# Performance work log

Hardware: AMD Instinct MI355X
Metric: run time of the kernel (lower is better)

## Reference

```python
import jax, jax.numpy as jnp
import numpy as np

B, S, D, H = 2, 2048, 1024, 16
DK = D // H


def setup_inputs() -> dict:
    key = jax.random.key(0)
    ks = jax.random.split(key, 8)
    q = jax.random.normal(ks[0], (B, S, D), dtype=jnp.float32)
    k = jax.random.normal(ks[1], (B, S, D), dtype=jnp.float32)
    v = jax.random.normal(ks[2], (B, S, D), dtype=jnp.float32)
    mask = jax.random.randint(ks[3], (B, 1, S, S), 0, 2, dtype=jnp.int32)
    sc = 1.0 / np.sqrt(D)
    Wq = jax.random.normal(ks[4], (D, D), dtype=jnp.float32) * sc
    Wk = jax.random.normal(ks[5], (D, D), dtype=jnp.float32) * sc
    Wv = jax.random.normal(ks[6], (D, D), dtype=jnp.float32) * sc
    Wo = jax.random.normal(ks[7], (D, D), dtype=jnp.float32) * sc
    return {"q": q, "k": k, "v": v, "mask": mask, "Wq": Wq, "Wk": Wk, "Wv": Wv, "Wo": Wo}


def reference(q, k, v, mask, Wq, Wk, Wv, Wo):
    # Linear projections (torch Linear: x @ W.T; bias=False). Weights here stored
    # as [D, D] applied as x @ W (equivalent parameterization).
    query = q @ Wq  # [B,S,D]
    key = k @ Wk
    value = v @ Wv
    # split heads -> [B,H,S,DK]
    query = query.reshape(B, S, H, DK).transpose(0, 2, 1, 3)
    key = key.reshape(B, S, H, DK).transpose(0, 2, 1, 3)
    value = value.reshape(B, S, H, DK).transpose(0, 2, 1, 3)
    scores = jnp.einsum('bhqd,bhkd->bhqk', query, key) / jnp.sqrt(jnp.float32(DK))
    scores = jnp.where(mask == 0, jnp.float32(-1e9), scores)
    probs = jax.nn.softmax(scores, axis=-1)  # dropout p=0.0 -> identity
    x = jnp.einsum('bhqk,bhkd->bhqd', probs, value)
    x = x.transpose(0, 2, 1, 3).reshape(B, S, D)
    return x @ Wo
```

## Files before the change

kernel.cpp:

```cpp
#include <hip/hip_runtime.h>
#include <hip/hip_bf16.h>
#include <math.h>

#define B_ 2
#define S_ 2048
#define D_ 1024
#define H_ 16
#define DK_ 64
#define SW_ (S_ / 64)

typedef unsigned short u16;
typedef unsigned int u32;
typedef unsigned long long u64;
typedef __attribute__((ext_vector_type(8))) short short8;
typedef __attribute__((ext_vector_type(4))) float float4_;
typedef __attribute__((ext_vector_type(4))) unsigned int uint4_;

static __device__ inline u16 f_to_bf16(float f) {
    union { float f; u32 i; } x; x.f = f;
    u32 r = x.i + 0x7fff + ((x.i >> 16) & 1);
    return (u16)(r >> 16);
}

static __device__ __forceinline__ u32 cvtpk(float a, float b) {
    u32 r;
    asm("v_cvt_pk_bf16_f32 %0, %1, %2" : "=v"(r) : "v"(a), "v"(b));
    return r;
}

static __device__ __forceinline__ float fast_exp2(float x) {
#if __has_builtin(__builtin_amdgcn_exp2f)
    return __builtin_amdgcn_exp2f(x);
#else
    return exp2f(x);
#endif
}

static __device__ inline void gl_lds16(const u16* g, u16* l) {
    __builtin_amdgcn_global_load_lds((const __attribute__((address_space(1))) void*)g,
                                     (__attribute__((address_space(3))) void*)l, 16, 0, 0);
}

__global__ __launch_bounds__(256) void prep(const float* __restrict__ q,
                                            const float* __restrict__ k,
                                            const float* __restrict__ v,
                                            const int* __restrict__ mask,
                                            const float* __restrict__ W0,
                                            const float* __restrict__ W1,
                                            const float* __restrict__ W2,
                                            const float* __restrict__ W3,
                                            u16* __restrict__ qb, u16* __restrict__ kb,
                                            u16* __restrict__ vb,
                                            u16* __restrict__ T0, u16* __restrict__ T1,
                                            u16* __restrict__ T2, u16* __restrict__ T3,
                                            u64* __restrict__ mpk) {
    __shared__ float tile[32][33];
    int gx = blockIdx.x, tid = threadIdx.x;
    if (gx < 6144) {
        int z = gx >> 11;
        int bx = gx & 2047;
        const float* s = (z == 0) ? q : ((z == 1) ? k : v);
        u16* d = (z == 0) ? qb : ((z == 1) ? kb : vb);
        int i = (bx * 256 + tid) * 8;
        #pragma unroll
        for (int j = 0; j < 8; ++j) d[i + j] = f_to_bf16(s[i + j]);
    } else if (gx < 10240) {
        int g2 = gx - 6144;
        int z = g2 >> 10;
        int rem = g2 & 1023;
        const float* W = (z == 0) ? W0 : ((z == 1) ? W1 : ((z == 2) ? W2 : W3));
        u16* Wt = (z == 0) ? T0 : ((z == 1) ? T1 : ((z == 2) ? T2 : T3));
        int k0 = (rem >> 5) * 32, n0 = (rem & 31) * 32;
        int tx = tid & 31, ty = tid >> 5;
        #pragma unroll
        for (int i2 = 0; i2 < 4; ++i2) {
            int row = ty + i2 * 8;
            tile[row][tx] = W[(size_t)(k0 + row) * D_ + n0 + tx];
        }
        __syncthreads();
        #pragma unroll
        for (int i2 = 0; i2 < 4; ++i2) {
            int row = ty + i2 * 8;
            Wt[(size_t)(n0 + row) * D_ + k0 + tx] = f_to_bf16(tile[tx][row]);
        }
    } else {
        int g3 = gx - 10240;
        int wv = (g3 * 256 + tid) >> 6;
        int lane = tid & 63;
        #pragma unroll
        for (int i2 = 0; i2 < 8; ++i2) {
            int wd = wv * 8 + i2;
            u64 bits = __ballot(mask[(size_t)wd * 64 + lane] != 0);
            if (lane == 0) mpk[wd] = bits;
        }
    }
}

static __device__ __forceinline__ void gemm128_body(u16* lds,
                                                    const u16* __restrict__ A,
                                                    const u16* __restrict__ Bt,
                                                    int K, float4_ (&acc)[4][4]) {
    u16* ldsA = lds;
    u16* ldsB = lds + 8192;
    int tm = blockIdx.x, tn = blockIdx.y;
    int t = threadIdx.x, l = t & 63;
    int w = t >> 6, wr = w >> 1, wc = w & 1;
    int colL = l & 15, grp = l >> 4;
    int sw4 = (grp ^ ((colL >> 1) & 3)) << 3;
    int f0 = t, f1 = t + 256;
    int row0 = f0 >> 2, kc0 = (((f0 & 3) ^ ((f0 >> 3) & 3)) << 3);
    int row1 = f1 >> 2, kc1 = (((f1 & 3) ^ ((f1 >> 3) & 3)) << 3);
    const u16* gA0 = A  + (size_t)(tm * 128 + row0) * K + kc0;
    const u16* gA1 = A  + (size_t)(tm * 128 + row1) * K + kc1;
    const u16* gB0 = Bt + (size_t)(tn * 128 + row0) * K + kc0;
    const u16* gB1 = Bt + (size_t)(tn * 128 + row1) * K + kc1;

    #pragma unroll
    for (int mi = 0; mi < 4; ++mi)
        #pragma unroll
        for (int ni = 0; ni < 4; ++ni)
            acc[mi][ni] = (float4_){0.f, 0.f, 0.f, 0.f};

    gl_lds16(gA0, ldsA + f0 * 8);
    gl_lds16(gA1, ldsA + f1 * 8);
    gl_lds16(gB0, ldsB + f0 * 8);
    gl_lds16(gB1, ldsB + f1 * 8);

    for (int k0 = 0; k0 < K; k0 += 32) {
        int cur = (k0 >> 5) & 1;
        if (k0 + 32 < K) {
            int nb = (cur ^ 1) * 4096;
            gl_lds16(gA0 + k0 + 32, ldsA + nb + f0 * 8);
            gl_lds16(gA1 + k0 + 32, ldsA + nb + f1 * 8);
            gl_lds16(gB0 + k0 + 32, ldsB + nb + f0 * 8);
            gl_lds16(gB1 + k0 + 32, ldsB + nb + f1 * 8);
            asm volatile("s_waitcnt vmcnt(4)" ::: "memory");
        } else {
            asm volatile("s_waitcnt vmcnt(0)" ::: "memory");
        }
        __builtin_amdgcn_s_barrier();
        const u16* cA = ldsA + cur * 4096;
        const u16* cB = ldsB + cur * 4096;
        short8 a[4], b[4];
        #pragma unroll
        for (int mi = 0; mi < 4; ++mi)
            a[mi] = *(const short8*)&cA[(wr * 64 + mi * 16 + colL) * 32 + sw4];
        #pragma unroll
        for (int ni = 0; ni < 4; ++ni)
            b[ni] = *(const short8*)&cB[(wc * 64 + ni * 16 + colL) * 32 + sw4];
        #pragma unroll
        for (int mi = 0; mi < 4; ++mi)
            #pragma unroll
            for (int ni = 0; ni < 4; ++ni)
                acc[mi][ni] = __builtin_amdgcn_mfma_f32_16x16x32_bf16(a[mi], b[ni], acc[mi][ni], 0, 0, 0);
        __builtin_amdgcn_s_barrier();
    }
}

__global__ __launch_bounds__(256, 3) void gemm_qkv(const u16* __restrict__ qb,
                                                   const u16* __restrict__ kb,
                                                   const u16* __restrict__ vb,
                                                   const u16* __restrict__ Wqt,
                                                   const u16* __restrict__ Wkt,
                                                   const u16* __restrict__ Wvt,
                                                   u16* __restrict__ Qp,
                                                   u16* __restrict__ Kp,
                                                   u16* __restrict__ Vt) {
    __shared__ u16 lds[16384];
    int z = blockIdx.z;
    const u16* A  = (z == 0) ? qb  : ((z == 1) ? kb  : vb);
    const u16* Bt = (z == 0) ? Wqt : ((z == 1) ? Wkt : Wvt);
    float4_ acc[4][4];
    gemm128_body(lds, A, Bt, D_, acc);

    int tm = blockIdx.x, tn = blockIdx.y;
    int t = threadIdx.x, l = t & 63;
    int w = t >> 6, wr = w >> 1, wc = w & 1;
    int colL = l & 15, grp = l >> 4;

    if (z < 2) {
        u16* Y = (z == 0) ? Qp : Kp;
        float sc = (z == 0) ? (0.125f * 1.44269504f) : 1.0f;
        #pragma unroll
        for (int mi = 0; mi < 4; ++mi)
            #pragma unroll
            for (int ni = 0; ni < 4; ++ni)
                #pragma unroll
                for (int r = 0; r < 4; ++r)
                    Y[(size_t)(tm * 128 + wr * 64 + mi * 16 + grp * 4 + r) * D_
                      + tn * 128 + wc * 64 + ni * 16 + colL] = f_to_bf16(acc[mi][ni][r] * sc);
    } else {
        int tok_base = tm * 128 + wr * 64;
        int bb = tok_base >> 11;
        int s_hi = tok_base & (S_ - 1);
        #pragma unroll
        for (int mi = 0; mi < 4; ++mi)
            #pragma unroll
            for (int ni = 0; ni < 4; ++ni) {
                int n  = tn * 128 + wc * 64 + ni * 16 + colL;
                int hh = n >> 6, dk = n & 63;
                u16* vp = Vt + ((size_t)(bb * H_ + hh) * DK_ + dk) * S_ + s_hi;
                #pragma unroll
                for (int r = 0; r < 4; ++r) {
                    int m = mi * 16 + grp * 4 + r;
                    int mp_ = ((m >> 5) & 1) * 32 + ((m >> 2) & 3) * 8 + ((m >> 4) & 1) * 4 + (m & 3);
                    vp[mp_] = f_to_bf16(acc[mi][ni][r]);
                }
            }
    }
}

__global__ __launch_bounds__(256, 3) void gemm_out(const u16* __restrict__ Xa,
                                                   const u16* __restrict__ Wot,
                                                   float* __restrict__ out) {
    __shared__ u16 lds[16384];
    float4_ acc[4][4];
    gemm128_body(lds, Xa, Wot, D_, acc);

    int tm = blockIdx.x, tn = blockIdx.y;
    int t = threadIdx.x, l = t & 63;
    int w = t >> 6, wr = w >> 1, wc = w & 1;
    int colL = l & 15, grp = l >> 4;
    #pragma unroll
    for (int mi = 0; mi < 4; ++mi)
        #pragma unroll
        for (int ni = 0; ni < 4; ++ni)
            #pragma unroll
            for (int r = 0; r < 4; ++r)
                out[(size_t)(tm * 128 + wr * 64 + mi * 16 + grp * 4 + r) * D_
                    + tn * 128 + wc * 64 + ni * 16 + colL] = acc[mi][ni][r];
}

__global__ __launch_bounds__(256, 2) void attn128(const u16* __restrict__ Qp,
                                                  const u16* __restrict__ Kp,
                                                  const u16* __restrict__ Vt,
                                                  const u64* __restrict__ mp,
                                                  u16* __restrict__ Xa) {
    __shared__ u16 ldsK[2 * 128 * 64];
    __shared__ u16 ldsV[2 * 2 * 64 * 64];

    int bid0 = blockIdx.x;
    int bid = ((bid0 & 7) << 6) | (bid0 >> 3);
    int qt = bid & 15, h = (bid >> 4) & 15, b = bid >> 8;
    int t = threadIdx.x, l = t & 63, w = t >> 6;
    int colL = l & 15, grp = l >> 4;

    const u16* qbA = Qp + (size_t)(b * S_ + qt * 128 + w * 32 + colL) * D_ + h * DK_;
    const u16* qbB = qbA + (size_t)16 * D_;
    short8 qfA0 = *(const short8*)(qbA + grp * 8);
    short8 qfA1 = *(const short8*)(qbA + 32 + grp * 8);
    short8 qfB0 = *(const short8*)(qbB + grp * 8);
    short8 qfB1 = *(const short8*)(qbB + 32 + grp * 8);

    const u16* gK[4];
    const u16* gV[4];
    int fofs[4];
    #pragma unroll
    for (int i = 0; i < 4; ++i) {
        int f = t + 256 * i;
        fofs[i] = f * 8;
        int krow = f >> 3, kch = (((f & 7) ^ (krow & 7)) << 3);
        gK[i] = Kp + (size_t)(b * S_ + krow) * D_ + h * DK_ + kch;
        int hreg = f >> 9, fp = f & 511;
        int vrow = fp >> 3, vch = (((fp & 7) ^ (vrow & 7)) << 3);
        gV[i] = Vt + ((size_t)(b * H_ + h) * DK_ + vrow) * S_ + hreg * 64 + vch;
    }

    int sw8 = (grp ^ (colL & 7)) << 3;

    short8 onesb;
    #pragma unroll
    for (int j = 0; j < 8; ++j) onesb[j] = (short)0x3F80;

    float4_ laccA = (float4_){0.f, 0.f, 0.f, 0.f};
    float4_ laccB = (float4_){0.f, 0.f, 0.f, 0.f};
    float4_ oA[4], oB[4];
    #pragma unroll
    for (int nt = 0; nt < 4; ++nt) {
        oA[nt] = (float4_){0.f, 0.f, 0.f, 0.f};
        oB[nt] = (float4_){0.f, 0.f, 0.f, 0.f};
    }

    const u64* mrA = mp + (size_t)(b * S_ + qt * 128 + w * 32 + colL) * SW_;
    const u64* mrB = mrA + (size_t)16 * SW_;

    #pragma unroll
    for (int i = 0; i < 4; ++i) {
        gl_lds16(gK[i], ldsK + fofs[i]);
        gl_lds16(gV[i], ldsV + fofs[i]);
    }

    for (int kt = 0; kt < S_; kt += 128) {
        int cur = (kt >> 7) & 1;

        u64 mwA0 = mrA[(kt >> 6)];
        u64 mwA1 = mrA[(kt >> 6) + 1];
        u64 mwB0 = mrB[(kt >> 6)];
        u64 mwB1 = mrB[(kt >> 6) + 1];

        if (kt + 128 < S_) {
            int nb = (cur ^ 1) * 8192;
            #pragma unroll
            for (int i = 0; i < 4; ++i) {
                gl_lds16(gK[i] + (size_t)(kt + 128) * D_, ldsK + nb + fofs[i]);
                gl_lds16(gV[i] + (kt + 128),              ldsV + nb + fofs[i]);
            }
            asm volatile("s_waitcnt vmcnt(12)" ::: "memory");
        } else {
            asm volatile("s_waitcnt vmcnt(4)" ::: "memory");
        }
        __builtin_amdgcn_s_barrier();

        const u16* K_ = ldsK + cur * 8192;
        const u16* V_ = ldsV + cur * 8192;

        float4_ sA[8], sB[8];
        __builtin_amdgcn_s_setprio(1);
        #pragma unroll
        for (int nt = 0; nt < 8; ++nt) {
            int ro = (nt * 16 + colL) * 64;
            short8 kf0 = *(const short8*)&K_[ro + sw8];
            short8 kf1 = *(const short8*)&K_[ro + (sw8 ^ 32)];
            sA[nt] = (float4_){0.f, 0.f, 0.f, 0.f};
            sA[nt] = __builtin_amdgcn_mfma_f32_16x16x32_bf16(kf0, qfA0, sA[nt], 0, 0, 0);
            sA[nt] = __builtin_amdgcn_mfma_f32_16x16x32_bf16(kf1, qfA1, sA[nt], 0, 0, 0);
            sB[nt] = (float4_){0.f, 0.f, 0.f, 0.f};
            sB[nt] = __builtin_amdgcn_mfma_f32_16x16x32_bf16(kf0, qfB0, sB[nt], 0, 0, 0);
            sB[nt] = __builtin_amdgcn_mfma_f32_16x16x32_bf16(kf1, qfB1, sB[nt], 0, 0, 0);
        }
        __builtin_amdgcn_s_setprio(0);

        u64 mshA0 = mwA0 >> (grp * 4), mshA1 = mwA1 >> (grp * 4);
        u64 mshB0 = mwB0 >> (grp * 4), mshB1 = mwB1 >> (grp * 4);
        #pragma unroll
        for (int nt = 0; nt < 8; ++nt) {
            u32 bitsA = ((u32)((nt < 4 ? mshA0 : mshA1) >> ((nt & 3) * 16))) & 15u;
            u32 bitsB = ((u32)((nt < 4 ? mshB0 : mshB1) >> ((nt & 3) * 16))) & 15u;
            #pragma unroll
            for (int r = 0; r < 4; ++r) {
                float pA = fast_exp2(sA[nt][r]);
                float pB = fast_exp2(sB[nt][r]);
                u32 keepA = 0u - ((bitsA >> r) & 1u);
                u32 keepB = 0u - ((bitsB >> r) & 1u);
                union { float f; u32 i; } ua, ub;
                ua.f = pA; ua.i &= keepA; sA[nt][r] = ua.f;
                ub.f = pB; ub.i &= keepB; sB[nt][r] = ub.f;
            }
        }

        short8 pfA[4], pfB[4];
        #pragma unroll
        for (int j = 0; j < 4; ++j) {
            uint4_ Ax = { cvtpk(sA[2 * j][0], sA[2 * j][1]), cvtpk(sA[2 * j][2], sA[2 * j][3]),
                          cvtpk(sA[2 * j + 1][0], sA[2 * j + 1][1]), cvtpk(sA[2 * j + 1][2], sA[2 * j + 1][3]) };
            pfA[j] = __builtin_bit_cast(short8, Ax);
            uint4_ Bx = { cvtpk(sB[2 * j][0], sB[2 * j][1]), cvtpk(sB[2 * j][2], sB[2 * j][3]),
                          cvtpk(sB[2 * j + 1][0], sB[2 * j + 1][1]), cvtpk(sB[2 * j + 1][2], sB[2 * j + 1][3]) };
            pfB[j] = __builtin_bit_cast(short8, Bx);
        }

        __builtin_amdgcn_s_setprio(1);
        #pragma unroll
        for (int nt = 0; nt < 4; ++nt) {
            int ro = (nt * 16 + colL) * 64;
            short8 vf0 = *(const short8*)&V_[ro + sw8];
            short8 vf1 = *(const short8*)&V_[ro + (sw8 ^ 32)];
            short8 vf2 = *(const short8*)&V_[4096 + ro + sw8];
            short8 vf3 = *(const short8*)&V_[4096 + ro + (sw8 ^ 32)];
            oA[nt] = __builtin_amdgcn_mfma_f32_16x16x32_bf16(pfA[0], vf0, oA[nt], 0, 0, 0);
            oA[nt] = __builtin_amdgcn_mfma_f32_16x16x32_bf16(pfA[1], vf1, oA[nt], 0, 0, 0);
            oA[nt] = __builtin_amdgcn_mfma_f32_16x16x32_bf16(pfA[2], vf2, oA[nt], 0, 0, 0);
            oA[nt] = __builtin_amdgcn_mfma_f32_16x16x32_bf16(pfA[3], vf3, oA[nt], 0, 0, 0);
            oB[nt] = __builtin_amdgcn_mfma_f32_16x16x32_bf16(pfB[0], vf0, oB[nt], 0, 0, 0);
            oB[nt] = __builtin_amdgcn_mfma_f32_16x16x32_bf16(pfB[1], vf1, oB[nt], 0, 0, 0);
            oB[nt] = __builtin_amdgcn_mfma_f32_16x16x32_bf16(pfB[2], vf2, oB[nt], 0, 0, 0);
            oB[nt] = __builtin_amdgcn_mfma_f32_16x16x32_bf16(pfB[3], vf3, oB[nt], 0, 0, 0);
        }
        laccA = __builtin_amdgcn_mfma_f32_16x16x32_bf16(pfA[0], onesb, laccA, 0, 0, 0);
        laccA = __builtin_amdgcn_mfma_f32_16x16x32_bf16(pfA[1], onesb, laccA, 0, 0, 0);
        laccA = __builtin_amdgcn_mfma_f32_16x16x32_bf16(pfA[2], onesb, laccA, 0, 0, 0);
        laccA = __builtin_amdgcn_mfma_f32_16x16x32_bf16(pfA[3], onesb, laccA, 0, 0, 0);
        laccB = __builtin_amdgcn_mfma_f32_16x16x32_bf16(pfB[0], onesb, laccB, 0, 0, 0);
        laccB = __builtin_amdgcn_mfma_f32_16x16x32_bf16(pfB[1], onesb, laccB, 0, 0, 0);
        laccB = __builtin_amdgcn_mfma_f32_16x16x32_bf16(pfB[2], onesb, laccB, 0, 0, 0);
        laccB = __builtin_amdgcn_mfma_f32_16x16x32_bf16(pfB[3], onesb, laccB, 0, 0, 0);
        __builtin_amdgcn_s_setprio(0);

        __builtin_amdgcn_s_barrier();
    }

    float invA[4], invB[4];
    #pragma unroll
    for (int r = 0; r < 4; ++r) {
        invA[r] = 1.f / laccA[r];
        invB[r] = 1.f / laccB[r];
    }

    u16* xoA = Xa + (size_t)(b * S_ + qt * 128 + w * 32 + grp * 4) * D_ + h * DK_;
    u16* xoB = xoA + (size_t)16 * D_;
    #pragma unroll
    for (int r = 0; r < 4; ++r)
        #pragma unroll
        for (int nt = 0; nt < 4; ++nt) {
            xoA[(size_t)r * D_ + nt * 16 + colL] = f_to_bf16(oA[nt][r] * invA[r]);
            xoB[(size_t)r * D_ + nt * 16 + colL] = f_to_bf16(oB[nt][r] * invB[r]);
        }
}

extern "C" void kernel_launch(void* const* d_in, const int* in_sizes, int n_in,
                              void* d_out, int out_size, void* d_ws, size_t ws_size,
                              hipStream_t stream) {
    const float* q    = (const float*)d_in[0];
    const float* k    = (const float*)d_in[1];
    const float* v    = (const float*)d_in[2];
    const int*   mask = (const int*)d_in[3];
    const float* Wq   = (const float*)d_in[4];
    const float* Wk   = (const float*)d_in[5];
    const float* Wv   = (const float*)d_in[6];
    const float* Wo   = (const float*)d_in[7];
    float* out = (float*)d_out;

    const int NQ = B_ * S_ * D_;
    const int NW = D_ * D_;

    u16* qb  = (u16*)d_ws;
    u16* kb  = qb  + NQ;
    u16* vb  = kb  + NQ;
    u16* Wqt = vb  + NQ;
    u16* Wkt = Wqt + NW;
    u16* Wvt = Wkt + NW;
    u16* Wot = Wvt + NW;
    u16* Qp  = Wot + NW;
    u16* Kp  = Qp  + NQ;
    u16* Vt  = Kp  + NQ;
    u16* Xa  = Vt  + NQ;
    u64* mpk = (u64*)(Xa + NQ);

    dim3 cblk(256);
    prep<<<14336, cblk, 0, stream>>>(q, k, v, mask, Wq, Wk, Wv, Wo,
                                     qb, kb, vb, Wqt, Wkt, Wvt, Wot, mpk);

    const int M = B_ * S_;
    gemm_qkv<<<dim3(M / 128, D_ / 128, 3), cblk, 0, stream>>>(qb, kb, vb, Wqt, Wkt, Wvt, Qp, Kp, Vt);

    attn128<<<B_ * H_ * (S_ / 128), cblk, 0, stream>>>(Qp, Kp, Vt, mpk, Xa);

    gemm_out<<<dim3(M / 128, D_ / 128), cblk, 0, stream>>>(Xa, Wot, out);
}
```

Measured before the change: 238.5 us.

## Vectorize input conversion, move mask packing into QKV GEMM, shrink output tiles

The fp32-to-bf16 conversion of q/k/v now uses 16-byte vector loads and stores with packed rounding instead of scalar element stores. The mask bit-packing moves out of the prep kernel into an extra z-slice of the QKV GEMM grid, so it runs alongside the projection blocks. The output GEMM switches to 64x128 tiles with its own double-buffered loop, doubling the block count to 512 to improve occupancy on the 1024-wide output projection. The trade-off is less reuse per block and added divergence and branching in the QKV kernel.

```diff
diff --git a/kernel.cpp b/kernel.cpp
--- a/kernel.cpp
+++ b/kernel.cpp
@@ -22,6 +22,13 @@
     return (u16)(r >> 16);
 }
 
+static __device__ __forceinline__ u32 packrne(float a, float b) {
+    union { float f; u32 i; } xa, xb; xa.f = a; xb.f = b;
+    u32 lo = (xa.i + 0x7fff + ((xa.i >> 16) & 1)) >> 16;
+    u32 hi = (xb.i + 0x7fff + ((xb.i >> 16) & 1)) & 0xffff0000u;
+    return lo | hi;
+}
+
 static __device__ __forceinline__ u32 cvtpk(float a, float b) {
     u32 r;
     asm("v_cvt_pk_bf16_f32 %0, %1, %2" : "=v"(r) : "v"(a), "v"(b));
@@ -44,7 +51,6 @@
 __global__ __launch_bounds__(256) void prep(const float* __restrict__ q,
                                             const float* __restrict__ k,
                                             const float* __restrict__ v,
-                                            const int* __restrict__ mask,
                                             const float* __restrict__ W0,
                                             const float* __restrict__ W1,
                                             const float* __restrict__ W2,
@@ -52,8 +58,7 @@
                                             u16* __restrict__ qb, u16* __restrict__ kb,
                                             u16* __restrict__ vb,
                                             u16* __restrict__ T0, u16* __restrict__ T1,
-                                            u16* __restrict__ T2, u16* __restrict__ T3,
-                                            u64* __restrict__ mpk) {
+                                            u16* __restrict__ T2, u16* __restrict__ T3) {
     __shared__ float tile[32][33];
     int gx = blockIdx.x, tid = threadIdx.x;
     if (gx < 6144) {
@@ -62,9 +67,12 @@
         const float* s = (z == 0) ? q : ((z == 1) ? k : v);
         u16* d = (z == 0) ? qb : ((z == 1) ? kb : vb);
         int i = (bx * 256 + tid) * 8;
-        #pragma unroll
-        for (int j = 0; j < 8; ++j) d[i + j] = f_to_bf16(s[i + j]);
-    } else if (gx < 10240) {
+        float4_ a0 = *(const float4_*)(s + i);
+        float4_ a1 = *(const float4_*)(s + i + 4);
+        uint4_ wv_ = { packrne(a0[0], a0[1]), packrne(a0[2], a0[3]),
+                       packrne(a1[0], a1[1]), packrne(a1[2], a1[3]) };
+        *(uint4_*)(d + i) = wv_;
+    } else {
         int g2 = gx - 6144;
         int z = g2 >> 10;
         int rem = g2 & 1023;
@@ -82,16 +90,6 @@
         for (int i2 = 0; i2 < 4; ++i2) {
             int row = ty + i2 * 8;
             Wt[(size_t)(n0 + row) * D_ + k0 + tx] = f_to_bf16(tile[tx][row]);
-        }
-    } else {
-        int g3 = gx - 10240;
-        int wv = (g3 * 256 + tid) >> 6;
-        int lane = tid & 63;
-        #pragma unroll
-        for (int i2 = 0; i2 < 8; ++i2) {
-            int wd = wv * 8 + i2;
-            u64 bits = __ballot(mask[(size_t)wd * 64 + lane] != 0);
-            if (lane == 0) mpk[wd] = bits;
         }
     }
 }
@@ -165,16 +163,37 @@
                                                    const u16* __restrict__ Wvt,
                                                    u16* __restrict__ Qp,
                                                    u16* __restrict__ Kp,
-                                                   u16* __restrict__ Vt) {
+                                                   u16* __restrict__ Vt,
+                                                   const int* __restrict__ mask,
+                                                   u64* __restrict__ mpk) {
     __shared__ u16 lds[16384];
     int z = blockIdx.z;
+    int tm = blockIdx.x, tn = blockIdx.y;
+    int t = threadIdx.x;
+
+    if (z == 3) {
+        int flat = tm * 8 + tn;
+        int w_ = t >> 6, lane = t & 63;
+        int base = flat * 512 + w_ * 128;
+        #pragma unroll 4
+        for (int it = 0; it < 16; ++it) {
+            int b2 = base + it * 8;
+            #pragma unroll
+            for (int i2 = 0; i2 < 8; ++i2) {
+                int wd = b2 + i2;
+                u64 bits = __ballot(mask[(size_t)wd * 64 + lane] != 0);
+                if (lane == 0) mpk[wd] = bits;
+            }
+        }
+        return;
+    }
+
     const u16* A  = (z == 0) ? qb  : ((z == 1) ? kb  : vb);
     const u16* Bt = (z == 0) ? Wqt : ((z == 1) ? Wkt : Wvt);
     float4_ acc[4][4];
     gemm128_body(lds, A, Bt, D_, acc);
 
-    int tm = blockIdx.x, tn = blockIdx.y;
-    int t = threadIdx.x, l = t & 63;
+    int l = t & 63;
     int w = t >> 6, wr = w >> 1, wc = w & 1;
     int colL = l & 15, grp = l >> 4;
 
@@ -210,24 +229,69 @@
     }
 }
 
-__global__ __launch_bounds__(256, 3) void gemm_out(const u16* __restrict__ Xa,
+__global__ __launch_bounds__(256, 2) void gemm_out(const u16* __restrict__ Xa,
                                                    const u16* __restrict__ Wot,
                                                    float* __restrict__ out) {
-    __shared__ u16 lds[16384];
-    float4_ acc[4][4];
-    gemm128_body(lds, Xa, Wot, D_, acc);
-
+    __shared__ u16 ldsA[2 * 2048];
+    __shared__ u16 ldsB[2 * 4096];
     int tm = blockIdx.x, tn = blockIdx.y;
     int t = threadIdx.x, l = t & 63;
     int w = t >> 6, wr = w >> 1, wc = w & 1;
     int colL = l & 15, grp = l >> 4;
-    #pragma unroll
-    for (int mi = 0; mi < 4; ++mi)
+    int sw4 = (grp ^ ((colL >> 1) & 3)) << 3;
+    int f0 = t, f1 = t + 256;
+    int row0 = f0 >> 2, kc0 = (((f0 & 3) ^ ((f0 >> 3) & 3)) << 3);
+    int row1 = f1 >> 2, kc1 = (((f1 & 3) ^ ((f1 >> 3) & 3)) << 3);
+    const u16* gA0 = Xa  + (size_t)(tm * 64 + row0) * D_ + kc0;
+    const u16* gB0 = Wot + (size_t)(tn * 128 + row0) * D_ + kc0;
+    const u16* gB1 = Wot + (size_t)(tn * 128 + row1) * D_ + kc1;
+
+    float4_ acc[2][4];
+    #pragma unroll
+    for (int mi = 0; mi < 2; ++mi)
         #pragma unroll
         for (int ni = 0; ni < 4; ++ni)
+            acc[mi][ni] = (float4_){0.f, 0.f, 0.f, 0.f};
+
+    gl_lds16(gA0, ldsA + f0 * 8);
+    gl_lds16(gB0, ldsB + f0 * 8);
+    gl_lds16(gB1, ldsB + f1 * 8);
+
+    for (int k0 = 0; k0 < D_; k0 += 32) {
+        int cur = (k0 >> 5) & 1;
+        if (k0 + 32 < D_) {
+            gl_lds16(gA0 + k0 + 32, ldsA + (cur ^ 1) * 2048 + f0 * 8);
+            gl_lds16(gB0 + k0 + 32, ldsB + (cur ^ 1) * 4096 + f0 * 8);
+            gl_lds16(gB1 + k0 + 32, ldsB + (cur ^ 1) * 4096 + f1 * 8);
+            asm volatile("s_waitcnt vmcnt(3)" ::: "memory");
+        } else {
+            asm volatile("s_waitcnt vmcnt(0)" ::: "memory");
+        }
+        __builtin_amdgcn_s_barrier();
+        const u16* cA = ldsA + cur * 2048;
+        const u16* cB = ldsB + cur * 4096;
+        short8 a[2], b[4];
+        #pragma unroll
+        for (int mi = 0; mi < 2; ++mi)
+            a[mi] = *(const short8*)&cA[(wr * 32 + mi * 16 + colL) * 32 + sw4];
+        #pragma unroll
+        for (int ni = 0; ni < 4; ++ni)
+            b[ni] = *(const short8*)&cB[(wc * 64 + ni * 16 + colL) * 32 + sw4];
+        #pragma unroll
+        for (int mi = 0; mi < 2; ++mi)
+            #pragma unroll
+            for (int ni = 0; ni < 4; ++ni)
+                acc[mi][ni] = __builtin_amdgcn_mfma_f32_16x16x32_bf16(a[mi], b[ni], acc[mi][ni], 0, 0, 0);
+        __builtin_amdgcn_s_barrier();
+    }
+
+    #pragma unroll
+    for (int mi = 0; mi < 2; ++mi)
+        #pragma unroll
+        for (int ni = 0; ni < 4; ++ni)
             #pragma unroll
             for (int r = 0; r < 4; ++r)
-                out[(size_t)(tm * 128 + wr * 64 + mi * 16 + grp * 4 + r) * D_
+                out[(size_t)(tm * 64 + wr * 32 + mi * 16 + grp * 4 + r) * D_
                     + tn * 128 + wc * 64 + ni * 16 + colL] = acc[mi][ni][r];
 }
 
@@ -437,13 +501,14 @@
     u64* mpk = (u64*)(Xa + NQ);
 
     dim3 cblk(256);
-    prep<<<14336, cblk, 0, stream>>>(q, k, v, mask, Wq, Wk, Wv, Wo,
-                                     qb, kb, vb, Wqt, Wkt, Wvt, Wot, mpk);
+    prep<<<10240, cblk, 0, stream>>>(q, k, v, Wq, Wk, Wv, Wo,
+                                     qb, kb, vb, Wqt, Wkt, Wvt, Wot);
 
     const int M = B_ * S_;
-    gemm_qkv<<<dim3(M / 128, D_ / 128, 3), cblk, 0, stream>>>(qb, kb, vb, Wqt, Wkt, Wvt, Qp, Kp, Vt);
+    gemm_qkv<<<dim3(M / 128, D_ / 128, 4), cblk, 0, stream>>>(qb, kb, vb, Wqt, Wkt, Wvt,
+                                                              Qp, Kp, Vt, mask, mpk);
 
     attn128<<<B_ * H_ * (S_ / 128), cblk, 0, stream>>>(Qp, Kp, Vt, mpk, Xa);
 
-    gemm_out<<<dim3(M / 128, D_ / 128), cblk, 0, stream>>>(Xa, Wot, out);
-}
+    gemm_out<<<dim3(M / 64, D_ / 128), cblk, 0, stream>>>(Xa, Wot, out);
+}
```

Result: slower. 283.5 us (+18.8%).
